# Kernel tuning notes

Measured on AMD Instinct MI355X. Metric: run time of the kernel, lower is better.

## Reference

```python
import jax, jax.numpy as jnp
import numpy as np
from jax import lax

INPUT_SIZE = 64
HIDDEN = 64
LAYERS = 8
B, T = 256, 2048


def setup_inputs() -> dict:
    key = jax.random.key(0)
    ks = jax.random.split(key, 10)
    s = 1.0 / np.sqrt(HIDDEN)  # PyTorch RNN init scale U(-1/sqrt(h), 1/sqrt(h))
    u = lambda k, shape: jax.random.uniform(k, shape, jnp.float32, -s, s)
    return {
        "x": jax.random.normal(ks[0], (B, T, INPUT_SIZE), jnp.float32),
        "h_state": jnp.zeros((LAYERS, B, HIDDEN), jnp.float32),
        "W_ih0": u(ks[1], (HIDDEN, INPUT_SIZE)),        # layer-0 input weights
        "W_ih": u(ks[2], (LAYERS - 1, HIDDEN, HIDDEN)), # layers 1..7 input weights
        "W_hh": u(ks[3], (LAYERS, HIDDEN, HIDDEN)),
        "b_ih": u(ks[4], (LAYERS, HIDDEN)),
        "b_hh": u(ks[5], (LAYERS, HIDDEN)),
        "W_out": u(ks[6], (1, HIDDEN)),
        "b_out": u(ks[7], (1,)),
    }


def reference(x, h_state, W_ih0, W_ih, W_hh, b_ih, b_hh, W_out, b_out):
    # Precompute layer-0 input projection for all timesteps (one big GEMM).
    x_proj = jnp.einsum("bti,hi->bth", x, W_ih0) + b_ih[0]  # [B,T,H]
    xt = jnp.transpose(x_proj, (1, 0, 2))  # [T,B,H]

    def step(h, x_t):
        # h: [LAYERS, B, H]; one timestep of the 8-layer tanh RNN stack
        new_h = []
        inp = None
        for l in range(LAYERS):
            if l == 0:
                pre = x_t + h[0] @ W_hh[0].T + b_hh[0]
            else:
                pre = inp @ W_ih[l - 1].T + b_ih[l] + h[l] @ W_hh[l].T + b_hh[l]
            inp = jnp.tanh(pre)
            new_h.append(inp)
        return jnp.stack(new_h), inp  # carry, top-layer output

    h_final, tops = lax.scan(step, h_state, xt)  # tops: [T,B,H]
    # Batched output projection (replaces the per-timestep Python loop)
    y = jnp.transpose(tops @ W_out.T + b_out, (1, 0, 2))  # [B,T,1]
    return (y, h_final)
```

## Files before the change

### kernel.cpp

```cpp
#include <hip/hip_runtime.h>

typedef _Float16 h2 __attribute__((ext_vector_type(2)));
typedef _Float16 h8 __attribute__((ext_vector_type(8)));
typedef __fp16   g2 __attribute__((ext_vector_type(2)));
typedef __fp16   g8 __attribute__((ext_vector_type(8)));
typedef float    f32x4 __attribute__((ext_vector_type(4)));

#define TT 2048
#define HH 64
#define NL 8
#define NB 256
#define G  16
#define NCH (TT/G)
#define NI  (NCH + NL)

#define PRP 20
#define NNS 84

union GU { g8 v; g2 p[4]; h8 h; };

#define PH_BASE(l, P) (((l)*2 + (P)) * 2048)
#define CH_OFF(j, c)  ((j)*128 + ((((c) ^ ((j)&7))) * 16))

__device__ __forceinline__ float tanh_fast(float v){
    float e = __expf(2.0f * v);
    float r = __builtin_amdgcn_rcpf(e + 1.0f);
    return fmaf(-2.0f, r, 1.0f);
}


#define INTERVAL(MM, P, XC, XN) { \
    const int mm = (MM); \
    const bool act = (unsigned)(mm - wv) < (unsigned)NCH; \
    if (wv == 0){ \
        if (mm + 1 < NCH){ \
            _Pragma("unroll") \
            for (int j = 0; j < G; ++j) \
                *(_Float16*)(BB + PH_BASE(0, 1-(P)) + j*128 + (((lane>>3)^(j&7))*16) + (lane&7)*2) = (_Float16)XC[j]; \
        } \
        if (mm + 2 < NCH){ \
            _Pragma("unroll") \
            for (int j = 0; j < G; ++j) \
                XN[j] = x[((size_t)b*TT + (size_t)(mm+2)*G + j)*HH + lane]; \
        } \
    } \
    if (wv == 7 && mm >= 8){ \
         \
        GU ha0, ha1; \
        ha0.h = *(const h8*)(BB + PH_BASE(8, P) + CH_OFF(nn, g)); \
        ha1.h = *(const h8*)(BB + PH_BASE(8, P) + CH_OFF(nn, 4+g)); \
        f32x4 ay = {0.f, 0.f, 0.f, 0.f}; \
        ay = __builtin_amdgcn_mfma_f32_16x16x32_f16(ha0.v, woutB[0].v, ay, 0, 0, 0); \
        ay = __builtin_amdgcn_mfma_f32_16x16x32_f16(ha1.v, woutB[1].v, ay, 0, 0, 0); \
        if (nn == 0){ \
            f32x4 st; \
            st[0] = ay[0] + bout; st[1] = ay[1] + bout; \
            st[2] = ay[2] + bout; st[3] = ay[3] + bout; \
            *(f32x4*)(yout + (size_t)b*TT + (size_t)(mm-8)*G + g*4) = st; \
        } \
    } \
    if (act){ \
        if (wv > 0){ \
            while (((volatile int*)prodF)[wv] < mm) __builtin_amdgcn_s_sleep(1); \
            asm volatile("" ::: "memory"); \
        } \
         \
        GU bx0, bx1; \
        bx0.h = *(const h8*)(BB + PH_BASE(wv, P) + CH_OFF(nn, g)); \
        bx1.h = *(const h8*)(BB + PH_BASE(wv, P) + CH_OFF(nn, 4+g)); \
        f32x4 xd0 = {bs[0],bs[0],bs[0],bs[0]}, xd1 = {bs[1],bs[1],bs[1],bs[1]}; \
        f32x4 xd2 = {bs[2],bs[2],bs[2],bs[2]}, xd3 = {bs[3],bs[3],bs[3],bs[3]}; \
        xd0 = __builtin_amdgcn_mfma_f32_16x16x32_f16(bx0.v, wihA[0][0].v, xd0, 0, 0, 0); \
        xd0 = __builtin_amdgcn_mfma_f32_16x16x32_f16(bx1.v, wihA[0][1].v, xd0, 0, 0, 0); \
        xd1 = __builtin_amdgcn_mfma_f32_16x16x32_f16(bx0.v, wihA[1][0].v, xd1, 0, 0, 0); \
        xd1 = __builtin_amdgcn_mfma_f32_16x16x32_f16(bx1.v, wihA[1][1].v, xd1, 0, 0, 0); \
        xd2 = __builtin_amdgcn_mfma_f32_16x16x32_f16(bx0.v, wihA[2][0].v, xd2, 0, 0, 0); \
        xd2 = __builtin_amdgcn_mfma_f32_16x16x32_f16(bx1.v, wihA[2][1].v, xd2, 0, 0, 0); \
        xd3 = __builtin_amdgcn_mfma_f32_16x16x32_f16(bx0.v, wihA[3][0].v, xd3, 0, 0, 0); \
        xd3 = __builtin_amdgcn_mfma_f32_16x16x32_f16(bx1.v, wihA[3][1].v, xd3, 0, 0, 0); \
         \
        asm volatile("" ::: "memory"); \
        ((volatile int*)consF)[wv] = mm; \
         \
        *(f32x4*)(preTf + (size_t)(wv*16+nn)*NNS + 0*PRP + g*4) = xd0; \
        *(f32x4*)(preTf + (size_t)(wv*16+nn)*NNS + 1*PRP + g*4) = xd1; \
        *(f32x4*)(preTf + (size_t)(wv*16+nn)*NNS + 2*PRP + g*4) = xd2; \
        *(f32x4*)(preTf + (size_t)(wv*16+nn)*NNS + 3*PRP + g*4) = xd3; \
        f32x4 prv0, prv1, prv2, prv3; \
        { \
            const float* pb = preTf + (size_t)(wv*16+nn)*NNS + g*PRP; \
            prv0 = *(const f32x4*)(pb);      prv1 = *(const f32x4*)(pb + 4); \
            prv2 = *(const f32x4*)(pb + 8);  prv3 = *(const f32x4*)(pb + 12); \
        } \
         \
        if (wv < 7){ \
            while (((volatile int*)consF)[wv+1] < mm-1) __builtin_amdgcn_s_sleep(1); \
            asm volatile("" ::: "memory"); \
        } \
         \
        _Pragma("unroll") \
        for (int j = 0; j < G; ++j){ \
            GU hA0, hA1; \
            if (j == 0){ hA0 = hp0; hA1 = hp1; } \
            else { \
                hA0.h = *(const h8*)(BB + PH_BASE(wv+1, 1-(P)) + CH_OFF(j-1, g)); \
                hA1.h = *(const h8*)(BB + PH_BASE(wv+1, 1-(P)) + CH_OFF(j-1, 4+g)); \
            } \
            const f32x4 zz = {0.f, 0.f, 0.f, 0.f}; \
            f32x4 a00 = __builtin_amdgcn_mfma_f32_16x16x32_f16(hA0.v, whhB[0][0].v, zz, 0, 0, 0); \
            f32x4 a01 = __builtin_amdgcn_mfma_f32_16x16x32_f16(hA1.v, whhB[0][1].v, zz, 0, 0, 0); \
            f32x4 a10 = __builtin_amdgcn_mfma_f32_16x16x32_f16(hA0.v, whhB[1][0].v, zz, 0, 0, 0); \
            f32x4 a11 = __builtin_amdgcn_mfma_f32_16x16x32_f16(hA1.v, whhB[1][1].v, zz, 0, 0, 0); \
            f32x4 a20 = __builtin_amdgcn_mfma_f32_16x16x32_f16(hA0.v, whhB[2][0].v, zz, 0, 0, 0); \
            f32x4 a21 = __builtin_amdgcn_mfma_f32_16x16x32_f16(hA1.v, whhB[2][1].v, zz, 0, 0, 0); \
            f32x4 a30 = __builtin_amdgcn_mfma_f32_16x16x32_f16(hA0.v, whhB[3][0].v, zz, 0, 0, 0); \
            f32x4 a31 = __builtin_amdgcn_mfma_f32_16x16x32_f16(hA1.v, whhB[3][1].v, zz, 0, 0, 0); \
            const float s0 = a00[0] + a01[0], s1 = a10[0] + a11[0]; \
            const float s2 = a20[0] + a21[0], s3 = a30[0] + a31[0]; \
            const float pa = (g & 2) ? ((g & 1) ? s3 : s2) : ((g & 1) ? s1 : s0); \
            const float prj = (j < 4) ? prv0[j&3] : (j < 8) ? prv1[j&3] \
                             : (j < 12) ? prv2[j&3] : prv3[j&3]; \
            const float hn = tanh_fast(pa + prj); \
            *(_Float16*)(BB + PH_BASE(wv+1, 1-(P)) + j*128 + (((lane>>3)^(j&7))*16) + (lane&7)*2) = (_Float16)hn; \
            if (j == G-1){ \
                hp0.h = *(const h8*)(BB + PH_BASE(wv+1, 1-(P)) + CH_OFF(G-1, g)); \
                hp1.h = *(const h8*)(BB + PH_BASE(wv+1, 1-(P)) + CH_OFF(G-1, 4+g)); \
            } \
            if (mm - wv == NCH-1 && j == G-1) \
                hout[((size_t)wv*NB + b)*HH + lane] = hn; \
        } \
         \
        asm volatile("" ::: "memory"); \
        ((volatile int*)prodF)[wv+1] = mm + 1; \
    } \
}

__global__ void __launch_bounds__(512) rnn_kernel(
    const float* __restrict__ x,
    const float* __restrict__ h_state,
    const float* __restrict__ W_ih0,
    const float* __restrict__ W_ih,
    const float* __restrict__ W_hh,
    const float* __restrict__ b_ih,
    const float* __restrict__ b_hh,
    const float* __restrict__ W_out,
    const float* __restrict__ b_out,
    float* __restrict__ out)
{
    __shared__ __attribute__((aligned(16))) _Float16 buf[(NL+1)*2*G*HH];
    __shared__ __attribute__((aligned(16))) float preT[NL*16*NNS];
    __shared__ int prodF[16];
    __shared__ int consF[16];
    char* BB = (char*)buf;
    float* preTf = preT;
    const int tid  = threadIdx.x;
    const int wv   = tid >> 6;
    const int lane = tid & 63;
    const int g    = lane >> 4;
    const int nn   = lane & 15;
    const size_t b = blockIdx.x;

    GU wihA[4][2], whhB[4][2];
    const float* Wi = (wv == 0) ? W_ih0 : (W_ih + (size_t)(wv-1)*HH*HH);
    const float* Wh = W_hh + (size_t)wv*HH*HH;
    #pragma unroll
    for (int t = 0; t < 4; ++t){
        #pragma unroll
        for (int kt = 0; kt < 2; ++kt){
            const float* pi = Wi + (size_t)(t*16 + nn)*HH + kt*32 + g*8;
            const float* ph = Wh + (size_t)(t*16 + nn)*HH + kt*32 + g*8;
            f32x4 i0 = *(const f32x4*)(pi), i1 = *(const f32x4*)(pi + 4);
            f32x4 h0 = *(const f32x4*)(ph), h1 = *(const f32x4*)(ph + 4);
            wihA[t][kt].p[0] = __builtin_amdgcn_cvt_pkrtz(i0[0], i0[1]);
            wihA[t][kt].p[1] = __builtin_amdgcn_cvt_pkrtz(i0[2], i0[3]);
            wihA[t][kt].p[2] = __builtin_amdgcn_cvt_pkrtz(i1[0], i1[1]);
            wihA[t][kt].p[3] = __builtin_amdgcn_cvt_pkrtz(i1[2], i1[3]);
            whhB[t][kt].p[0] = __builtin_amdgcn_cvt_pkrtz(h0[0], h0[1]);
            whhB[t][kt].p[1] = __builtin_amdgcn_cvt_pkrtz(h0[2], h0[3]);
            whhB[t][kt].p[2] = __builtin_amdgcn_cvt_pkrtz(h1[0], h1[1]);
            whhB[t][kt].p[3] = __builtin_amdgcn_cvt_pkrtz(h1[2], h1[3]);
        }
    }
    float bs[4];
    #pragma unroll
    for (int t = 0; t < 4; ++t)
        bs[t] = b_ih[wv*HH + t*16 + nn] + b_hh[wv*HH + t*16 + nn];
    float bout = b_out[0];

    GU woutB[2];
    if (wv == 7){
        #pragma unroll
        for (int kt = 0; kt < 2; ++kt)
            #pragma unroll
            for (int q = 0; q < 4; ++q)
                woutB[kt].p[q] = __builtin_amdgcn_cvt_pkrtz(
                    W_out[kt*32 + g*8 + q*2], W_out[kt*32 + g*8 + q*2 + 1]);
    }

    for (int i = tid; i < (NL+1)*2*G*HH; i += 512) buf[i] = (_Float16)0.f;
    if (tid < 16){
        prodF[tid] = 0;
        consF[tid] = tid - 2;
    }
    __syncthreads();
    *(_Float16*)(BB + PH_BASE(wv+1, 1-(wv&1)) + (G-1)*128 + (((lane>>3)^((G-1)&7))*16) + (lane&7)*2)
        = (_Float16)h_state[((size_t)wv*NB + b)*HH + lane];
    float xa[G], xb[G];
    if (wv == 0){
        #pragma unroll
        for (int j = 0; j < G; ++j){
            *(_Float16*)(BB + PH_BASE(0, 1) + j*128 + (((lane>>3)^(j&7))*16) + (lane&7)*2)
                = (_Float16)x[((size_t)b*TT + j)*HH + lane];
            xa[j] = x[((size_t)b*TT + G + j)*HH + lane];
        }
    }
    __syncthreads();

    GU hp0, hp1;
    hp0.h = *(const h8*)(BB + PH_BASE(wv+1, 1-(wv&1)) + CH_OFF(G-1, g));
    hp1.h = *(const h8*)(BB + PH_BASE(wv+1, 1-(wv&1)) + CH_OFF(G-1, 4+g));

    float* yout = out;
    float* hout = out + (size_t)NB*TT;

    for (int m2 = 0; m2 < NI; m2 += 2){
        INTERVAL(m2,     1, xa, xb)
        INTERVAL(m2 + 1, 0, xb, xa)
    }
}

extern "C" void kernel_launch(void* const* d_in, const int* in_sizes, int n_in,
                              void* d_out, int out_size, void* d_ws, size_t ws_size,
                              hipStream_t stream) {
    (void)in_sizes; (void)n_in; (void)d_ws; (void)ws_size; (void)out_size;
    const float* x       = (const float*)d_in[0];
    const float* h_state = (const float*)d_in[1];
    const float* W_ih0   = (const float*)d_in[2];
    const float* W_ih    = (const float*)d_in[3];
    const float* W_hh    = (const float*)d_in[4];
    const float* b_ih    = (const float*)d_in[5];
    const float* b_hh    = (const float*)d_in[6];
    const float* W_out   = (const float*)d_in[7];
    const float* b_out   = (const float*)d_in[8];
    float* out = (float*)d_out;

    rnn_kernel<<<dim3(NB), dim3(512), 0, stream>>>(
        x, h_state, W_ih0, W_ih, W_hh, b_ih, b_hh, W_out, b_out, out);
}
```

Measured before the change: 479.9 us.

## Double chunk size and stream layer-0 input via async global-to-LDS loads

Measured after the change: 433.9 us. 1.11x faster.

```diff
diff --git a/kernel.cpp b/kernel.cpp
--- a/kernel.cpp
+++ b/kernel.cpp
@@ -10,17 +10,21 @@
 #define HH 64
 #define NL 8
 #define NB 256
-#define G  16
+#define G  32
 #define NCH (TT/G)
 #define NI  (NCH + NL)
 
-#define PRP 20
-#define NNS 84
-
 union GU { g8 v; g2 p[4]; h8 h; };
 
-#define PH_BASE(l, P) (((l)*2 + (P)) * 2048)
-#define CH_OFF(j, c)  ((j)*128 + ((((c) ^ ((j)&7))) * 16))
+#define BUFB(idx, P) ((((idx)*2 + (P))) * 4096)
+#define CH_OFF(j, c) ((j)*128 + ((((c) ^ ((j)&7))) * 16))
+
+#define PRP 36
+#define NNS 148
+#define PRE_L (16*NNS)
+
+#define XQ_ROW 68
+#define XQ_PH  (32*XQ_ROW)
 
 __device__ __forceinline__ float tanh_fast(float v){
     float e = __expf(2.0f * v);
@@ -28,36 +32,66 @@
     return fmaf(-2.0f, r, 1.0f);
 }
 
-
-#define INTERVAL(MM, P, XC, XN) { \
+__device__ __forceinline__ void gload_lds4(const float* g, float* l){
+    __builtin_amdgcn_global_load_lds(
+        (const __attribute__((address_space(1))) void*)g,
+        (__attribute__((address_space(3))) void*)l, 4, 0, 0);
+}
+
+
+#define XPROJ(bx0_, bx1_, off16) { \
+    f32x4 x0 = {bs[0],bs[0],bs[0],bs[0]}, x1 = {bs[1],bs[1],bs[1],bs[1]}; \
+    f32x4 x2 = {bs[2],bs[2],bs[2],bs[2]}, x3 = {bs[3],bs[3],bs[3],bs[3]}; \
+    x0 = __builtin_amdgcn_mfma_f32_16x16x32_f16(bx0_.v, wihA[0][0].v, x0, 0, 0, 0); \
+    x0 = __builtin_amdgcn_mfma_f32_16x16x32_f16(bx1_.v, wihA[0][1].v, x0, 0, 0, 0); \
+    x1 = __builtin_amdgcn_mfma_f32_16x16x32_f16(bx0_.v, wihA[1][0].v, x1, 0, 0, 0); \
+    x1 = __builtin_amdgcn_mfma_f32_16x16x32_f16(bx1_.v, wihA[1][1].v, x1, 0, 0, 0); \
+    x2 = __builtin_amdgcn_mfma_f32_16x16x32_f16(bx0_.v, wihA[2][0].v, x2, 0, 0, 0); \
+    x2 = __builtin_amdgcn_mfma_f32_16x16x32_f16(bx1_.v, wihA[2][1].v, x2, 0, 0, 0); \
+    x3 = __builtin_amdgcn_mfma_f32_16x16x32_f16(bx0_.v, wihA[3][0].v, x3, 0, 0, 0); \
+    x3 = __builtin_amdgcn_mfma_f32_16x16x32_f16(bx1_.v, wihA[3][1].v, x3, 0, 0, 0); \
+    *(f32x4*)(preW + nn*NNS + 0*PRP + (off16) + gq) = x0; \
+    *(f32x4*)(preW + nn*NNS + 1*PRP + (off16) + gq) = x1; \
+    *(f32x4*)(preW + nn*NNS + 2*PRP + (off16) + gq) = x2; \
+    *(f32x4*)(preW + nn*NNS + 3*PRP + (off16) + gq) = x3; \
+}
+
+#define XQREAD(bx0_, bx1_, xrp) { \
+    f32x4 q0 = *(const f32x4*)((xrp) + g*8); \
+    f32x4 q1 = *(const f32x4*)((xrp) + g*8 + 4); \
+    f32x4 q2 = *(const f32x4*)((xrp) + 32 + g*8); \
+    f32x4 q3 = *(const f32x4*)((xrp) + 36 + g*8); \
+    bx0_.p[0] = __builtin_amdgcn_cvt_pkrtz(q0[0], q0[1]); \
+    bx0_.p[1] = __builtin_amdgcn_cvt_pkrtz(q0[2], q0[3]); \
+    bx0_.p[2] = __builtin_amdgcn_cvt_pkrtz(q1[0], q1[1]); \
+    bx0_.p[3] = __builtin_amdgcn_cvt_pkrtz(q1[2], q1[3]); \
+    bx1_.p[0] = __builtin_amdgcn_cvt_pkrtz(q2[0], q2[1]); \
+    bx1_.p[1] = __builtin_amdgcn_cvt_pkrtz(q2[2], q2[3]); \
+    bx1_.p[2] = __builtin_amdgcn_cvt_pkrtz(q3[0], q3[1]); \
+    bx1_.p[3] = __builtin_amdgcn_cvt_pkrtz(q3[2], q3[3]); \
+}
+
+#define YPROJ(slotrow, ofs, PP) { \
+    GU ya0, ya1; \
+    ya0.h = *(const h8*)(BB + BUFB(7, PP) + CH_OFF((slotrow), g)); \
+    ya1.h = *(const h8*)(BB + BUFB(7, PP) + CH_OFF((slotrow), 4+g)); \
+    f32x4 ay = {0.f, 0.f, 0.f, 0.f}; \
+    ay = __builtin_amdgcn_mfma_f32_16x16x32_f16(ya0.v, woutB[0].v, ay, 0, 0, 0); \
+    ay = __builtin_amdgcn_mfma_f32_16x16x32_f16(ya1.v, woutB[1].v, ay, 0, 0, 0); \
+    if (nn == 0){ \
+        f32x4 st; \
+        st[0] = ay[0] + bout; st[1] = ay[1] + bout; \
+        st[2] = ay[2] + bout; st[3] = ay[3] + bout; \
+        *(f32x4*)(yout + (size_t)b*TT + (size_t)(mm-8)*G + (ofs) + g*4) = st; \
+    } \
+}
+
+#define INTERVAL(MM, P) { \
     const int mm = (MM); \
     const bool act = (unsigned)(mm - wv) < (unsigned)NCH; \
-    if (wv == 0){ \
-        if (mm + 1 < NCH){ \
-            _Pragma("unroll") \
-            for (int j = 0; j < G; ++j) \
-                *(_Float16*)(BB + PH_BASE(0, 1-(P)) + j*128 + (((lane>>3)^(j&7))*16) + (lane&7)*2) = (_Float16)XC[j]; \
-        } \
-        if (mm + 2 < NCH){ \
-            _Pragma("unroll") \
-            for (int j = 0; j < G; ++j) \
-                XN[j] = x[((size_t)b*TT + (size_t)(mm+2)*G + j)*HH + lane]; \
-        } \
-    } \
     if (wv == 7 && mm >= 8){ \
-         \
-        GU ha0, ha1; \
-        ha0.h = *(const h8*)(BB + PH_BASE(8, P) + CH_OFF(nn, g)); \
-        ha1.h = *(const h8*)(BB + PH_BASE(8, P) + CH_OFF(nn, 4+g)); \
-        f32x4 ay = {0.f, 0.f, 0.f, 0.f}; \
-        ay = __builtin_amdgcn_mfma_f32_16x16x32_f16(ha0.v, woutB[0].v, ay, 0, 0, 0); \
-        ay = __builtin_amdgcn_mfma_f32_16x16x32_f16(ha1.v, woutB[1].v, ay, 0, 0, 0); \
-        if (nn == 0){ \
-            f32x4 st; \
-            st[0] = ay[0] + bout; st[1] = ay[1] + bout; \
-            st[2] = ay[2] + bout; st[3] = ay[3] + bout; \
-            *(f32x4*)(yout + (size_t)b*TT + (size_t)(mm-8)*G + g*4) = st; \
-        } \
+        YPROJ(nn, 0, P) \
+        YPROJ(16+nn, 16, P) \
     } \
     if (act){ \
         if (wv > 0){ \
@@ -65,46 +99,45 @@
             asm volatile("" ::: "memory"); \
         } \
          \
-        GU bx0, bx1; \
-        bx0.h = *(const h8*)(BB + PH_BASE(wv, P) + CH_OFF(nn, g)); \
-        bx1.h = *(const h8*)(BB + PH_BASE(wv, P) + CH_OFF(nn, 4+g)); \
-        f32x4 xd0 = {bs[0],bs[0],bs[0],bs[0]}, xd1 = {bs[1],bs[1],bs[1],bs[1]}; \
-        f32x4 xd2 = {bs[2],bs[2],bs[2],bs[2]}, xd3 = {bs[3],bs[3],bs[3],bs[3]}; \
-        xd0 = __builtin_amdgcn_mfma_f32_16x16x32_f16(bx0.v, wihA[0][0].v, xd0, 0, 0, 0); \
-        xd0 = __builtin_amdgcn_mfma_f32_16x16x32_f16(bx1.v, wihA[0][1].v, xd0, 0, 0, 0); \
-        xd1 = __builtin_amdgcn_mfma_f32_16x16x32_f16(bx0.v, wihA[1][0].v, xd1, 0, 0, 0); \
-        xd1 = __builtin_amdgcn_mfma_f32_16x16x32_f16(bx1.v, wihA[1][1].v, xd1, 0, 0, 0); \
-        xd2 = __builtin_amdgcn_mfma_f32_16x16x32_f16(bx0.v, wihA[2][0].v, xd2, 0, 0, 0); \
-        xd2 = __builtin_amdgcn_mfma_f32_16x16x32_f16(bx1.v, wihA[2][1].v, xd2, 0, 0, 0); \
-        xd3 = __builtin_amdgcn_mfma_f32_16x16x32_f16(bx0.v, wihA[3][0].v, xd3, 0, 0, 0); \
-        xd3 = __builtin_amdgcn_mfma_f32_16x16x32_f16(bx1.v, wihA[3][1].v, xd3, 0, 0, 0); \
-         \
+        GU bxA0, bxA1, bxB0, bxB1; \
+        if (wv == 0){ \
+            asm volatile("s_waitcnt vmcnt(0)" ::: "memory"); \
+            XQREAD(bxA0, bxA1, xq + (mm&1)*XQ_PH + nn*XQ_ROW) \
+            XQREAD(bxB0, bxB1, xq + (mm&1)*XQ_PH + (16+nn)*XQ_ROW) \
+            if (mm + 1 < NCH){ \
+                const float* gx = x + ((size_t)b*TT + (size_t)(mm+1)*G)*HH + lane; \
+                float* lq = xq + (1-(mm&1))*XQ_PH; \
+                _Pragma("unroll") \
+                for (int j = 0; j < G; ++j) \
+                    gload_lds4(gx + j*HH, lq + j*XQ_ROW); \
+            } \
+        } else { \
+            bxA0.h = *(const h8*)(BB + BUFB(wv-1, P) + CH_OFF(nn, g)); \
+            bxA1.h = *(const h8*)(BB + BUFB(wv-1, P) + CH_OFF(nn, 4+g)); \
+            bxB0.h = *(const h8*)(BB + BUFB(wv-1, P) + CH_OFF(16+nn, g)); \
+            bxB1.h = *(const h8*)(BB + BUFB(wv-1, P) + CH_OFF(16+nn, 4+g)); \
+        } \
+        XPROJ(bxA0, bxA1, 0) \
+        XPROJ(bxB0, bxB1, 16) \
         asm volatile("" ::: "memory"); \
         ((volatile int*)consF)[wv] = mm; \
-         \
-        *(f32x4*)(preTf + (size_t)(wv*16+nn)*NNS + 0*PRP + g*4) = xd0; \
-        *(f32x4*)(preTf + (size_t)(wv*16+nn)*NNS + 1*PRP + g*4) = xd1; \
-        *(f32x4*)(preTf + (size_t)(wv*16+nn)*NNS + 2*PRP + g*4) = xd2; \
-        *(f32x4*)(preTf + (size_t)(wv*16+nn)*NNS + 3*PRP + g*4) = xd3; \
-        f32x4 prv0, prv1, prv2, prv3; \
-        { \
-            const float* pb = preTf + (size_t)(wv*16+nn)*NNS + g*PRP; \
-            prv0 = *(const f32x4*)(pb);      prv1 = *(const f32x4*)(pb + 4); \
-            prv2 = *(const f32x4*)(pb + 8);  prv3 = *(const f32x4*)(pb + 12); \
-        } \
-         \
         if (wv < 7){ \
             while (((volatile int*)consF)[wv+1] < mm-1) __builtin_amdgcn_s_sleep(1); \
             asm volatile("" ::: "memory"); \
         } \
+         \
+         \
+        const float* pb = preW + nn*NNS + g*PRP; \
+        f32x4 prv0 = *(const f32x4*)(pb);      f32x4 prv1 = *(const f32x4*)(pb + 4); \
+        f32x4 prv2 = *(const f32x4*)(pb + 8);  f32x4 prv3 = *(const f32x4*)(pb + 12); \
          \
         _Pragma("unroll") \
         for (int j = 0; j < G; ++j){ \
             GU hA0, hA1; \
             if (j == 0){ hA0 = hp0; hA1 = hp1; } \
             else { \
-                hA0.h = *(const h8*)(BB + PH_BASE(wv+1, 1-(P)) + CH_OFF(j-1, g)); \
-                hA1.h = *(const h8*)(BB + PH_BASE(wv+1, 1-(P)) + CH_OFF(j-1, 4+g)); \
+                hA0.h = *(const h8*)(BB + BUFB(wv, 1-(P)) + CH_OFF(j-1, g)); \
+                hA1.h = *(const h8*)(BB + BUFB(wv, 1-(P)) + CH_OFF(j-1, 4+g)); \
             } \
             const f32x4 zz = {0.f, 0.f, 0.f, 0.f}; \
             f32x4 a00 = __builtin_amdgcn_mfma_f32_16x16x32_f16(hA0.v, whhB[0][0].v, zz, 0, 0, 0); \
@@ -118,23 +151,29 @@
             const float s0 = a00[0] + a01[0], s1 = a10[0] + a11[0]; \
             const float s2 = a20[0] + a21[0], s3 = a30[0] + a31[0]; \
             const float pa = (g & 2) ? ((g & 1) ? s3 : s2) : ((g & 1) ? s1 : s0); \
-            const float prj = (j < 4) ? prv0[j&3] : (j < 8) ? prv1[j&3] \
-                             : (j < 12) ? prv2[j&3] : prv3[j&3]; \
+            float prj; \
+            { const int q = (j >> 2) & 3; \
+              prj = (q == 0) ? prv0[j&3] : (q == 1) ? prv1[j&3] \
+                  : (q == 2) ? prv2[j&3] : prv3[j&3]; } \
             const float hn = tanh_fast(pa + prj); \
-            *(_Float16*)(BB + PH_BASE(wv+1, 1-(P)) + j*128 + (((lane>>3)^(j&7))*16) + (lane&7)*2) = (_Float16)hn; \
+            *(_Float16*)(BB + BUFB(wv, 1-(P)) + j*128 + (((lane>>3)^(j&7))*16) + (lane&7)*2) = (_Float16)hn; \
+            if (j == 4)  prv0 = *(const f32x4*)(pb + 16); \
+            if (j == 8)  prv1 = *(const f32x4*)(pb + 20); \
+            if (j == 12) prv2 = *(const f32x4*)(pb + 24); \
+            if (j == 16) prv3 = *(const f32x4*)(pb + 28); \
             if (j == G-1){ \
-                hp0.h = *(const h8*)(BB + PH_BASE(wv+1, 1-(P)) + CH_OFF(G-1, g)); \
-                hp1.h = *(const h8*)(BB + PH_BASE(wv+1, 1-(P)) + CH_OFF(G-1, 4+g)); \
+                hp0.h = *(const h8*)(BB + BUFB(wv, 1-(P)) + CH_OFF(G-1, g)); \
+                hp1.h = *(const h8*)(BB + BUFB(wv, 1-(P)) + CH_OFF(G-1, 4+g)); \
+                if (mm - wv == NCH-1) \
+                    hout[((size_t)wv*NB + b)*HH + lane] = hn; \
             } \
-            if (mm - wv == NCH-1 && j == G-1) \
-                hout[((size_t)wv*NB + b)*HH + lane] = hn; \
-        } \
-         \
+        } \
         asm volatile("" ::: "memory"); \
         ((volatile int*)prodF)[wv+1] = mm + 1; \
     } \
 }
 
+__attribute__((amdgpu_waves_per_eu(2, 2)))
 __global__ void __launch_bounds__(512) rnn_kernel(
     const float* __restrict__ x,
     const float* __restrict__ h_state,
@@ -147,18 +186,20 @@
     const float* __restrict__ b_out,
     float* __restrict__ out)
 {
-    __shared__ __attribute__((aligned(16))) _Float16 buf[(NL+1)*2*G*HH];
-    __shared__ __attribute__((aligned(16))) float preT[NL*16*NNS];
+    __shared__ __attribute__((aligned(16))) _Float16 buf[8*2*G*HH];
+    __shared__ __attribute__((aligned(16))) float pre[NL*PRE_L];
+    __shared__ __attribute__((aligned(16))) float xq[2*XQ_PH];
     __shared__ int prodF[16];
     __shared__ int consF[16];
     char* BB = (char*)buf;
-    float* preTf = preT;
     const int tid  = threadIdx.x;
     const int wv   = tid >> 6;
     const int lane = tid & 63;
     const int g    = lane >> 4;
     const int nn   = lane & 15;
+    const int gq   = g*4;
     const size_t b = blockIdx.x;
+    float* preW = pre + (size_t)wv*PRE_L;
 
     GU wihA[4][2], whhB[4][2];
     const float* Wi = (wv == 0) ? W_ih0 : (W_ih + (size_t)(wv-1)*HH*HH);
@@ -197,35 +238,32 @@
                     W_out[kt*32 + g*8 + q*2], W_out[kt*32 + g*8 + q*2 + 1]);
     }
 
-    for (int i = tid; i < (NL+1)*2*G*HH; i += 512) buf[i] = (_Float16)0.f;
+    for (int i = tid; i < 8*2*G*HH; i += 512) buf[i] = (_Float16)0.f;
     if (tid < 16){
         prodF[tid] = 0;
         consF[tid] = tid - 2;
     }
     __syncthreads();
-    *(_Float16*)(BB + PH_BASE(wv+1, 1-(wv&1)) + (G-1)*128 + (((lane>>3)^((G-1)&7))*16) + (lane&7)*2)
+    *(_Float16*)(BB + BUFB(wv, 1-(wv&1)) + (G-1)*128 + (((lane>>3)^((G-1)&7))*16) + (lane&7)*2)
         = (_Float16)h_state[((size_t)wv*NB + b)*HH + lane];
-    float xa[G], xb[G];
     if (wv == 0){
+        const float* gx = x + (size_t)b*TT*HH + lane;
         #pragma unroll
-        for (int j = 0; j < G; ++j){
-            *(_Float16*)(BB + PH_BASE(0, 1) + j*128 + (((lane>>3)^(j&7))*16) + (lane&7)*2)
-                = (_Float16)x[((size_t)b*TT + j)*HH + lane];
-            xa[j] = x[((size_t)b*TT + G + j)*HH + lane];
-        }
+        for (int j = 0; j < G; ++j)
+            gload_lds4(gx + j*HH, xq + j*XQ_ROW);
     }
     __syncthreads();
 
     GU hp0, hp1;
-    hp0.h = *(const h8*)(BB + PH_BASE(wv+1, 1-(wv&1)) + CH_OFF(G-1, g));
-    hp1.h = *(const h8*)(BB + PH_BASE(wv+1, 1-(wv&1)) + CH_OFF(G-1, 4+g));
+    hp0.h = *(const h8*)(BB + BUFB(wv, 1-(wv&1)) + CH_OFF(G-1, g));
+    hp1.h = *(const h8*)(BB + BUFB(wv, 1-(wv&1)) + CH_OFF(G-1, 4+g));
 
     float* yout = out;
     float* hout = out + (size_t)NB*TT;
 
     for (int m2 = 0; m2 < NI; m2 += 2){
-        INTERVAL(m2,     1, xa, xb)
-        INTERVAL(m2 + 1, 0, xb, xa)
+        INTERVAL(m2,     1)
+        INTERVAL(m2 + 1, 0)
     }
 }
 
```
